# Kernel optimization log

Measured on AMD Instinct MI355X. Metric: run time of the kernel, lower is better.

The kernel has to match this reference:

```python
import jax, jax.numpy as jnp
import numpy as np

N_NODES = 100000
N_EDGES = 1600000
D_IN = 64
D_HID = 128
BN_EPS = 1e-5


def setup_inputs() -> dict:
    key = jax.random.key(0)
    ks = jax.random.split(key, 8)
    x = jax.random.normal(ks[0], (N_NODES, D_IN), dtype=jnp.float32)
    edge_index = jax.random.randint(ks[1], (2, N_EDGES), 0, N_NODES, dtype=jnp.int64)
    # MLP params (Linear stores W as [out, in]; we keep [in, out] for x @ W)
    s1 = 1.0 / np.sqrt(D_IN)
    s2 = 1.0 / np.sqrt(D_HID)
    W1 = jax.random.uniform(ks[2], (D_IN, D_HID), minval=-s1, maxval=s1, dtype=jnp.float32)
    b1 = jax.random.uniform(ks[3], (D_HID,), minval=-s1, maxval=s1, dtype=jnp.float32)
    W2 = jax.random.uniform(ks[4], (D_HID, D_HID), minval=-s2, maxval=s2, dtype=jnp.float32)
    b2 = jax.random.uniform(ks[5], (D_HID,), minval=-s2, maxval=s2, dtype=jnp.float32)
    gamma = jnp.ones((D_HID,), dtype=jnp.float32)
    beta = jnp.zeros((D_HID,), dtype=jnp.float32)
    return {"x": x, "edge_index": edge_index, "W1": W1, "b1": b1,
            "W2": W2, "b2": b2, "gamma": gamma, "beta": beta}


def reference(x, edge_index, W1, b1, W2, b2, gamma, beta):
    src, dst = edge_index[0], edge_index[1]
    # GIN sum aggregation: agg[i] = sum_{(j->i) in E} x[j]
    agg = jax.ops.segment_sum(x[src], dst, num_segments=N_NODES)
    h = x + agg  # eps = 0 (GINConv default)
    # 2-layer MLP with ReLU
    h = jax.nn.relu(h @ W1 + b1)
    h = h @ W2 + b2
    # outer ReLU
    h = jax.nn.relu(h)
    # BatchNorm1d (training mode: biased batch statistics over nodes)
    mean = jnp.mean(h, axis=0)
    var = jnp.var(h, axis=0)
    h = (h - mean) * jax.lax.rsqrt(var + BN_EPS) * gamma + beta
    return h
```

## Files before the change

### kernel.cpp

```cpp
#include <hip/hip_runtime.h>
#include <hip/hip_fp16.h>

#define N_NODES 100000
#define N_EDGES 1600000
#define D_IN 64
#define D_HID 128
#define NBINS 196
#define NBLK 200
#define EPB 8000
#define FCAP 10240

typedef __attribute__((ext_vector_type(8))) _Float16 half8;
typedef __attribute__((ext_vector_type(4))) float f32x4;

__device__ inline float2 h2f(unsigned u) {
    __half2 h = __builtin_bit_cast(__half2, u);
    return __half22float2(h);
}
__device__ inline unsigned f2h(float a, float b) {
    __half2 h = __floats2half2_rn(a, b);
    return __builtin_bit_cast(unsigned, h);
}

__global__ __launch_bounds__(256) void k_xhalf(const float4* __restrict__ x4,
                                               uint2* __restrict__ xh2) {
    int i = blockIdx.x * 256 + threadIdx.x;
    float4 v = x4[i];
    uint2 o;
    o.x = f2h(v.x, v.y);
    o.y = f2h(v.z, v.w);
    xh2[i] = o;
}

__global__ __launch_bounds__(256) void k_pcount(const int* __restrict__ dst,
                                                int* __restrict__ pbh) {
    __shared__ int hist[NBINS];
    int t = threadIdx.x, b = blockIdx.x;
    if (t < NBINS) hist[t] = 0;
    __syncthreads();
    for (int i = t; i < EPB; i += 256)
        atomicAdd(&hist[dst[b * EPB + i] >> 9], 1);
    __syncthreads();
    if (t < NBINS) pbh[t * NBLK + b] = hist[t];
}

__global__ void k_pscan(const int* __restrict__ pbh, int* __restrict__ pbo,
                        int* __restrict__ binstart, int* __restrict__ offs) {
    __shared__ int part[256];
    const int TOT = NBINS * NBLK;
    int t = threadIdx.x;
    int lo = t * 154, hi = lo + 154 < TOT ? lo + 154 : TOT;
    int s = 0;
    for (int i = lo; i < hi; ++i) s += pbh[i];
    part[t] = s;
    __syncthreads();
    for (int off = 1; off < 256; off <<= 1) {
        int val = part[t];
        int add = (t >= off) ? part[t - off] : 0;
        __syncthreads();
        part[t] = val + add;
        __syncthreads();
    }
    int run = t ? part[t - 1] : 0;
    for (int i = lo; i < hi; ++i) {
        int v = pbh[i];
        pbo[i] = run;
        if ((i % NBLK) == 0) binstart[i / NBLK] = run;
        run += v;
    }
    if (t == 0) { binstart[NBINS] = N_EDGES; offs[N_NODES] = N_EDGES; }
}

__global__ __launch_bounds__(256) void k_pscatter(const int* __restrict__ src,
                                                  const int* __restrict__ dst,
                                                  const int* __restrict__ pbo,
                                                  unsigned* __restrict__ packed) {
    __shared__ int cur[NBINS];
    int t = threadIdx.x, b = blockIdx.x;
    if (t < NBINS) cur[t] = pbo[t * NBLK + b];
    __syncthreads();
    for (int i = t; i < EPB; i += 256) {
        int e = b * EPB + i;
        int d = dst[e];
        int bin = d >> 9;
        int p = atomicAdd(&cur[bin], 1);
        packed[p] = ((unsigned)(d & 511) << 17) | (unsigned)src[e];
    }
}

__global__ __launch_bounds__(256) void k_fsort(const unsigned* __restrict__ packed,
                                               const int* __restrict__ binstart,
                                               int* __restrict__ offs,
                                               int* __restrict__ srcs) {
    __shared__ int nh[512];
    __shared__ int cur[512];
    __shared__ int part[256];
    __shared__ int stage[FCAP];
    int t = threadIdx.x, bin = blockIdx.x;
    int base = binstart[bin];
    int n = binstart[bin + 1] - base;
    nh[t] = 0; nh[t + 256] = 0;
    __syncthreads();
    for (int i = t; i < n; i += 256)
        atomicAdd(&nh[packed[base + i] >> 17], 1);
    __syncthreads();
    int a0 = nh[2 * t], a1 = nh[2 * t + 1];
    part[t] = a0 + a1;
    __syncthreads();
    for (int off = 1; off < 256; off <<= 1) {
        int val = part[t];
        int add = (t >= off) ? part[t - off] : 0;
        __syncthreads();
        part[t] = val + add;
        __syncthreads();
    }
    int excl = t ? part[t - 1] : 0;
    cur[2 * t] = excl;
    cur[2 * t + 1] = excl + a0;
    int node0 = bin * 512 + 2 * t;
    if (node0 < N_NODES) offs[node0] = base + excl;
    if (node0 + 1 < N_NODES) offs[node0 + 1] = base + excl + a0;
    __syncthreads();
    for (int i = t; i < n; i += 256) {
        unsigned u = packed[base + i];
        int dl = u >> 17;
        int s = u & 0x1FFFF;
        int p = atomicAdd(&cur[dl], 1);
        if (p < FCAP) stage[p] = s;
        else srcs[base + p] = s;
    }
    __syncthreads();
    int m = n < FCAP ? n : FCAP;
    for (int i = t; i < m; i += 256) srcs[base + i] = stage[i];
}

__global__ __launch_bounds__(256) void k_gather(const unsigned* __restrict__ xh,
                                                const int* __restrict__ offs,
                                                const int* __restrict__ srcs,
                                                unsigned* __restrict__ aggh) {
    int wid = (blockIdx.x * 256 + threadIdx.x) >> 6;
    int lane = threadIdx.x & 63;
    int half = lane >> 5, c = lane & 31;
    int beg = offs[wid], end = offs[wid + 1];
    float2 sum;
    if (half == 0) sum = h2f(xh[(size_t)wid * 32 + c]);
    else sum = make_float2(0.f, 0.f);
    int e = beg;
    for (; e + 4 <= end; e += 4) {
        int i0 = e + half, i1 = e + 2 + half;
        int s0 = srcs[i0], s1 = srcs[i1];
        float2 v0 = h2f(xh[(size_t)s0 * 32 + c]);
        float2 v1 = h2f(xh[(size_t)s1 * 32 + c]);
        sum.x += v0.x + v1.x;
        sum.y += v0.y + v1.y;
    }
    for (; e < end; e += 2) {
        int idx = e + half;
        if (idx < end) {
            float2 v = h2f(xh[(size_t)srcs[idx] * 32 + c]);
            sum.x += v.x; sum.y += v.y;
        }
    }
    sum.x += __shfl_xor(sum.x, 32);
    sum.y += __shfl_xor(sum.y, 32);
    if (half == 0) aggh[(size_t)wid * 32 + c] = f2h(sum.x, sum.y);
}

__global__ __launch_bounds__(256) void k_pack(const float* __restrict__ W1,
                                              const float* __restrict__ W2,
                                              _Float16* __restrict__ W1p,
                                              _Float16* __restrict__ W2p) {
    int t = blockIdx.x * 256 + threadIdx.x;
    if (t < 1024) {
        int l = t & 63;
        int row = ((t >> 9) & 1) * 32 + (l >> 4) * 8;
        int col = ((t >> 6) & 7) * 16 + (l & 15);
#pragma unroll
        for (int i = 0; i < 8; ++i)
            W1p[t * 8 + i] = (_Float16)W1[(row + i) * 128 + col];
    } else {
        int s = t - 1024;
        int l = s & 63;
        int row = (s >> 9) * 32 + (l >> 4) * 8;
        int col = ((s >> 6) & 7) * 16 + (l & 15);
#pragma unroll
        for (int i = 0; i < 8; ++i)
            W2p[s * 8 + i] = (_Float16)W2[(row + i) * 128 + col];
    }
}

__global__ __launch_bounds__(256) void k_gemm1(const _Float16* __restrict__ A,
                                               const _Float16* __restrict__ Wp,
                                               const float* __restrict__ bias,
                                               _Float16* __restrict__ H) {
    int lane = threadIdx.x & 63, wv = threadIdx.x >> 6;
    int row0 = blockIdx.x * 64 + wv * 16;
    int ar = row0 + (lane & 15);
    if (ar > N_NODES - 1) ar = N_NODES - 1;
    int ac = (lane >> 4) * 8;
    half8 a0 = *(const half8*)&A[(size_t)ar * 64 + ac];
    half8 a1 = *(const half8*)&A[(size_t)ar * 64 + 32 + ac];
    f32x4 acc[8];
#pragma unroll
    for (int ct = 0; ct < 8; ++ct) {
        half8 w0 = *(const half8*)&Wp[(size_t)(ct * 64 + lane) * 8];
        half8 w1 = *(const half8*)&Wp[(size_t)(512 + ct * 64 + lane) * 8];
        f32x4 c = {0.f, 0.f, 0.f, 0.f};
        c = __builtin_amdgcn_mfma_f32_16x16x32_f16(a0, w0, c, 0, 0, 0);
        c = __builtin_amdgcn_mfma_f32_16x16x32_f16(a1, w1, c, 0, 0, 0);
        acc[ct] = c;
    }
    int g = lane >> 4, cl = lane & 15;
#pragma unroll
    for (int ct = 0; ct < 8; ++ct) {
        int col = ct * 16 + cl;
        float b = bias[col];
#pragma unroll
        for (int r = 0; r < 4; ++r) {
            int row = row0 + g * 4 + r;
            if (row < N_NODES) {
                float v = fmaxf(acc[ct][r] + b, 0.f);
                H[(size_t)row * 128 + col] = (_Float16)v;
            }
        }
    }
}

__global__ __launch_bounds__(256) void k_gemm2(const _Float16* __restrict__ A,
                                               const _Float16* __restrict__ Wp,
                                               const float* __restrict__ bias,
                                               float* __restrict__ OUT,
                                               float* __restrict__ stats) {
    __shared__ float sred[4][256];
    int lane = threadIdx.x & 63, wv = threadIdx.x >> 6;
    int row0 = blockIdx.x * 64 + wv * 16;
    int ar = row0 + (lane & 15);
    if (ar > N_NODES - 1) ar = N_NODES - 1;
    int ac = (lane >> 4) * 8;
    half8 a[4];
#pragma unroll
    for (int kt = 0; kt < 4; ++kt)
        a[kt] = *(const half8*)&A[(size_t)ar * 128 + kt * 32 + ac];
    int g = lane >> 4, cl = lane & 15;
#pragma unroll
    for (int ct = 0; ct < 8; ++ct) {
        f32x4 c = {0.f, 0.f, 0.f, 0.f};
#pragma unroll
        for (int kt = 0; kt < 4; ++kt) {
            half8 w = *(const half8*)&Wp[(size_t)((kt * 8 + ct) * 64 + lane) * 8];
            c = __builtin_amdgcn_mfma_f32_16x16x32_f16(a[kt], w, c, 0, 0, 0);
        }
        int col = ct * 16 + cl;
        float b = bias[col];
        float s = 0.f, q = 0.f;
#pragma unroll
        for (int r = 0; r < 4; ++r) {
            int row = row0 + g * 4 + r;
            float v = fmaxf(c[r] + b, 0.f);
            if (row < N_NODES) {
                OUT[(size_t)row * 128 + col] = v;
                s += v; q += v * v;
            }
        }
        s += __shfl_xor(s, 16); s += __shfl_xor(s, 32);
        q += __shfl_xor(q, 16); q += __shfl_xor(q, 32);
        if (g == 0) { sred[wv][col] = s; sred[wv][128 + col] = q; }
    }
    __syncthreads();
    int tid = threadIdx.x;
    float v = sred[0][tid] + sred[1][tid] + sred[2][tid] + sred[3][tid];
    unsafeAtomicAdd(&stats[tid], v);
}

__global__ void k_finalize(const float* __restrict__ stats,
                           const float* __restrict__ gamma,
                           const float* __restrict__ beta,
                           float* __restrict__ ss) {
    int c = threadIdx.x;
    float mean = stats[c] * (1.0f / N_NODES);
    float var = stats[128 + c] * (1.0f / N_NODES) - mean * mean;
    float scale = gamma[c] * rsqrtf(var + 1e-5f);
    ss[c] = scale;
    ss[128 + c] = beta[c] - mean * scale;
}

__global__ __launch_bounds__(256) void k_bn(float4* __restrict__ out,
                                            const float4* __restrict__ ss) {
    int stride = gridDim.x * 256;
    for (int f = blockIdx.x * 256 + threadIdx.x; f < N_NODES * 32; f += stride) {
        int c4 = f & 31;
        float4 sc = ss[c4];
        float4 sh = ss[32 + c4];
        float4 v = out[f];
        v.x = v.x * sc.x + sh.x;
        v.y = v.y * sc.y + sh.y;
        v.z = v.z * sc.z + sh.z;
        v.w = v.w * sc.w + sh.w;
        out[f] = v;
    }
}

extern "C" void kernel_launch(void* const* d_in, const int* in_sizes, int n_in,
                              void* d_out, int out_size, void* d_ws, size_t ws_size,
                              hipStream_t stream) {
    const float* x     = (const float*)d_in[0];
    const int*   ei    = (const int*)d_in[1];
    const float* W1    = (const float*)d_in[2];
    const float* b1    = (const float*)d_in[3];
    const float* W2    = (const float*)d_in[4];
    const float* b2    = (const float*)d_in[5];
    const float* gamma = (const float*)d_in[6];
    const float* beta  = (const float*)d_in[7];
    float* out = (float*)d_out;

    char* w = (char*)d_ws;
    unsigned* xh   = (unsigned*)w;  w += (size_t)N_NODES * 32 * 4;
    unsigned* aggh = (unsigned*)w;  w += (size_t)N_NODES * 32 * 4;
    _Float16* h1h  = (_Float16*)w;  w += (size_t)N_NODES * D_HID * 2;
    unsigned* packed = (unsigned*)w; w += (size_t)N_EDGES * 4;
    int* srcs      = (int*)w;       w += (size_t)N_EDGES * 4;
    int* offs      = (int*)w;       w += (N_NODES + 1) * 4;
    int* pbh       = (int*)w;       w += NBINS * NBLK * 4;
    int* pbo       = (int*)w;       w += NBINS * NBLK * 4;
    int* binstart  = (int*)w;       w += (NBINS + 1) * 4;
    float* stats   = (float*)w;     w += 1024;
    float* ss      = (float*)w;     w += 1024;
    _Float16* W1p  = (_Float16*)w;  w += 16384;
    _Float16* W2p  = (_Float16*)w;  w += 32768;

    const int* src = ei;
    const int* dst = ei + N_EDGES;

    (void)hipMemsetAsync(stats, 0, 256 * sizeof(float), stream);

    k_pack    <<<12, 256, 0, stream>>>(W1, W2, W1p, W2p);
    k_xhalf   <<<N_NODES * 64 / 4 / 256, 256, 0, stream>>>((const float4*)x, (uint2*)xh);
    k_pcount  <<<NBLK, 256, 0, stream>>>(dst, pbh);
    k_pscan   <<<1, 256, 0, stream>>>(pbh, pbo, binstart, offs);
    k_pscatter<<<NBLK, 256, 0, stream>>>(src, dst, pbo, packed);
    k_fsort   <<<NBINS, 256, 0, stream>>>(packed, binstart, offs, srcs);
    k_gather  <<<N_NODES / 4, 256, 0, stream>>>(xh, offs, srcs, aggh);

    k_gemm1<<<(N_NODES + 63) / 64, 256, 0, stream>>>((const _Float16*)aggh, W1p, b1, h1h);
    k_gemm2<<<(N_NODES + 63) / 64, 256, 0, stream>>>(h1h, W2p, b2, out, stats);
    k_finalize<<<1, 128, 0, stream>>>(stats, gamma, beta, ss);
    k_bn<<<2048, 256, 0, stream>>>((float4*)out, (const float4*)ss);
}
```

Measured before the change: 383.5 us.

## Fuse both MLP GEMMs through LDS and store pre-BN output as fp16

Merges the two GEMM kernels into one. The first layer's ReLU output is staged per wave in padded shared memory instead of a global fp16 buffer, which removes a 25.6MB write and read of the hidden activations and one launch. The pre-BatchNorm activations are also written as fp16 to a workspace buffer, and the BN kernel converts them back to fp32. This halves that intermediate traffic but rounds the values to fp16 before normalisation, which costs some accuracy.

```diff
diff --git a/kernel.cpp b/kernel.cpp
--- a/kernel.cpp
+++ b/kernel.cpp
@@ -9,6 +9,7 @@
 #define NBLK 200
 #define EPB 8000
 #define FCAP 10240
+#define LROW 136
 
 typedef __attribute__((ext_vector_type(8))) _Float16 half8;
 typedef __attribute__((ext_vector_type(4))) float f32x4;
@@ -189,76 +190,61 @@
     }
 }
 
-__global__ __launch_bounds__(256) void k_gemm1(const _Float16* __restrict__ A,
-                                               const _Float16* __restrict__ Wp,
-                                               const float* __restrict__ bias,
-                                               _Float16* __restrict__ H) {
-    int lane = threadIdx.x & 63, wv = threadIdx.x >> 6;
-    int row0 = blockIdx.x * 64 + wv * 16;
-    int ar = row0 + (lane & 15);
-    if (ar > N_NODES - 1) ar = N_NODES - 1;
-    int ac = (lane >> 4) * 8;
-    half8 a0 = *(const half8*)&A[(size_t)ar * 64 + ac];
-    half8 a1 = *(const half8*)&A[(size_t)ar * 64 + 32 + ac];
-    f32x4 acc[8];
-#pragma unroll
-    for (int ct = 0; ct < 8; ++ct) {
-        half8 w0 = *(const half8*)&Wp[(size_t)(ct * 64 + lane) * 8];
-        half8 w1 = *(const half8*)&Wp[(size_t)(512 + ct * 64 + lane) * 8];
-        f32x4 c = {0.f, 0.f, 0.f, 0.f};
-        c = __builtin_amdgcn_mfma_f32_16x16x32_f16(a0, w0, c, 0, 0, 0);
-        c = __builtin_amdgcn_mfma_f32_16x16x32_f16(a1, w1, c, 0, 0, 0);
-        acc[ct] = c;
-    }
-    int g = lane >> 4, cl = lane & 15;
-#pragma unroll
-    for (int ct = 0; ct < 8; ++ct) {
-        int col = ct * 16 + cl;
-        float b = bias[col];
-#pragma unroll
-        for (int r = 0; r < 4; ++r) {
-            int row = row0 + g * 4 + r;
-            if (row < N_NODES) {
-                float v = fmaxf(acc[ct][r] + b, 0.f);
-                H[(size_t)row * 128 + col] = (_Float16)v;
-            }
-        }
-    }
-}
-
-__global__ __launch_bounds__(256) void k_gemm2(const _Float16* __restrict__ A,
-                                               const _Float16* __restrict__ Wp,
-                                               const float* __restrict__ bias,
-                                               float* __restrict__ OUT,
-                                               float* __restrict__ stats) {
+__global__ __launch_bounds__(256) void k_mlp(const _Float16* __restrict__ A,
+                                             const _Float16* __restrict__ W1p,
+                                             const float* __restrict__ b1,
+                                             const _Float16* __restrict__ W2p,
+                                             const float* __restrict__ b2,
+                                             _Float16* __restrict__ OUTH,
+                                             float* __restrict__ stats) {
+    __shared__ _Float16 h1l[4][16 * LROW];
     __shared__ float sred[4][256];
     int lane = threadIdx.x & 63, wv = threadIdx.x >> 6;
     int row0 = blockIdx.x * 64 + wv * 16;
     int ar = row0 + (lane & 15);
     if (ar > N_NODES - 1) ar = N_NODES - 1;
     int ac = (lane >> 4) * 8;
-    half8 a[4];
+    int g = lane >> 4, cl = lane & 15;
+
+    half8 a0 = *(const half8*)&A[(size_t)ar * 64 + ac];
+    half8 a1 = *(const half8*)&A[(size_t)ar * 64 + 32 + ac];
+#pragma unroll
+    for (int ct = 0; ct < 8; ++ct) {
+        half8 w0 = *(const half8*)&W1p[(size_t)(ct * 64 + lane) * 8];
+        half8 w1 = *(const half8*)&W1p[(size_t)(512 + ct * 64 + lane) * 8];
+        f32x4 c = {0.f, 0.f, 0.f, 0.f};
+        c = __builtin_amdgcn_mfma_f32_16x16x32_f16(a0, w0, c, 0, 0, 0);
+        c = __builtin_amdgcn_mfma_f32_16x16x32_f16(a1, w1, c, 0, 0, 0);
+        float b = b1[ct * 16 + cl];
+#pragma unroll
+        for (int r = 0; r < 4; ++r) {
+            float v = fmaxf(c[r] + b, 0.f);
+            h1l[wv][(g * 4 + r) * LROW + ct * 16 + cl] = (_Float16)v;
+        }
+    }
+    __syncthreads();
+
+    half8 a2[4];
 #pragma unroll
     for (int kt = 0; kt < 4; ++kt)
-        a[kt] = *(const half8*)&A[(size_t)ar * 128 + kt * 32 + ac];
-    int g = lane >> 4, cl = lane & 15;
+        a2[kt] = *(const half8*)&h1l[wv][(lane & 15) * LROW + kt * 32 + ac];
 #pragma unroll
     for (int ct = 0; ct < 8; ++ct) {
         f32x4 c = {0.f, 0.f, 0.f, 0.f};
 #pragma unroll
         for (int kt = 0; kt < 4; ++kt) {
-            half8 w = *(const half8*)&Wp[(size_t)((kt * 8 + ct) * 64 + lane) * 8];
-            c = __builtin_amdgcn_mfma_f32_16x16x32_f16(a[kt], w, c, 0, 0, 0);
+            half8 w = *(const half8*)&W2p[(size_t)((kt * 8 + ct) * 64 + lane) * 8];
+            c = __builtin_amdgcn_mfma_f32_16x16x32_f16(a2[kt], w, c, 0, 0, 0);
         }
         int col = ct * 16 + cl;
-        float b = bias[col];
+        float b = b2[col];
         float s = 0.f, q = 0.f;
 #pragma unroll
         for (int r = 0; r < 4; ++r) {
             int row = row0 + g * 4 + r;
             float v = fmaxf(c[r] + b, 0.f);
             if (row < N_NODES) {
-                OUT[(size_t)row * 128 + col] = v;
+                OUTH[(size_t)row * 128 + col] = (_Float16)v;
                 s += v; q += v * v;
             }
         }
@@ -284,18 +270,21 @@
     ss[128 + c] = beta[c] - mean * scale;
 }
 
-__global__ __launch_bounds__(256) void k_bn(float4* __restrict__ out,
+__global__ __launch_bounds__(256) void k_bn(const uint2* __restrict__ outh,
+                                            float4* __restrict__ out,
                                             const float4* __restrict__ ss) {
     int stride = gridDim.x * 256;
     for (int f = blockIdx.x * 256 + threadIdx.x; f < N_NODES * 32; f += stride) {
         int c4 = f & 31;
         float4 sc = ss[c4];
         float4 sh = ss[32 + c4];
-        float4 v = out[f];
-        v.x = v.x * sc.x + sh.x;
-        v.y = v.y * sc.y + sh.y;
-        v.z = v.z * sc.z + sh.z;
-        v.w = v.w * sc.w + sh.w;
+        uint2 u = outh[f];
+        float2 lo = h2f(u.x), hi = h2f(u.y);
+        float4 v;
+        v.x = lo.x * sc.x + sh.x;
+        v.y = lo.y * sc.y + sh.y;
+        v.z = hi.x * sc.z + sh.z;
+        v.w = hi.y * sc.w + sh.w;
         out[f] = v;
     }
 }
@@ -316,7 +305,7 @@
     char* w = (char*)d_ws;
     unsigned* xh   = (unsigned*)w;  w += (size_t)N_NODES * 32 * 4;
     unsigned* aggh = (unsigned*)w;  w += (size_t)N_NODES * 32 * 4;
-    _Float16* h1h  = (_Float16*)w;  w += (size_t)N_NODES * D_HID * 2;
+    _Float16* outh = (_Float16*)w;  w += (size_t)N_NODES * D_HID * 2;
     unsigned* packed = (unsigned*)w; w += (size_t)N_EDGES * 4;
     int* srcs      = (int*)w;       w += (size_t)N_EDGES * 4;
     int* offs      = (int*)w;       w += (N_NODES + 1) * 4;
@@ -341,8 +330,8 @@
     k_fsort   <<<NBINS, 256, 0, stream>>>(packed, binstart, offs, srcs);
     k_gather  <<<N_NODES / 4, 256, 0, stream>>>(xh, offs, srcs, aggh);
 
-    k_gemm1<<<(N_NODES + 63) / 64, 256, 0, stream>>>((const _Float16*)aggh, W1p, b1, h1h);
-    k_gemm2<<<(N_NODES + 63) / 64, 256, 0, stream>>>(h1h, W2p, b2, out, stats);
+    k_mlp<<<(N_NODES + 63) / 64, 256, 0, stream>>>((const _Float16*)aggh,
+                                                   W1p, b1, W2p, b2, outh, stats);
     k_finalize<<<1, 128, 0, stream>>>(stats, gamma, beta, ss);
-    k_bn<<<2048, 256, 0, stream>>>((float4*)out, (const float4*)ss);
-}
+    k_bn<<<2048, 256, 0, stream>>>((const uint2*)outh, (float4*)out, (const float4*)ss);
+}
```

Result: faster. 362.4 us (-5.5%).
